# Kernel tuning notes

Measured on AMD Instinct MI355X. Metric: run time of the kernel, lower is better.

## Reference

```python
import jax, jax.numpy as jnp
import numpy as np

D_PAIR = 128
C = 128
EPS = 1e-5

def _ln(x, g, b):
    mu = jnp.mean(x, axis=-1, keepdims=True)
    var = jnp.var(x, axis=-1, keepdims=True)
    return (x - mu) * jax.lax.rsqrt(var + EPS) * g + b

def setup_inputs() -> dict:
    key = jax.random.key(0)
    ks = jax.random.split(key, 8)
    B, N, d, c = 1, 512, D_PAIR, C
    glorot = lambda k, fo, fi: jax.random.uniform(k, (fo, fi), jnp.float32,
                                                  -1.0, 1.0) * np.sqrt(6.0 / (fi + fo))
    return {
        "Z_raw": jax.random.normal(ks[0], (B, N, N, d), jnp.float32),
        "Z_mask_row": jnp.ones((B, N, N), jnp.float32),
        "ln1_g": jnp.ones((d,), jnp.float32),
        "ln1_b": jnp.zeros((d,), jnp.float32),
        "W_lr": glorot(ks[1], 2 * c, d),
        "b_lr": jnp.zeros((2 * c,), jnp.float32),
        "W_gate": jnp.zeros((2 * c, d), jnp.float32),   # initializer='zeros'
        "b_gate": jnp.ones((2 * c,), jnp.float32),      # bias_init=1.0
        "W_og": jnp.zeros((d, d), jnp.float32),
        "b_og": jnp.ones((d,), jnp.float32),
        "ln2_g": jnp.ones((c,), jnp.float32),
        "ln2_b": jnp.zeros((c,), jnp.float32),
        "W_out": jnp.zeros((d, d), jnp.float32),        # no bias
        "out_bias": jnp.zeros((d,), jnp.float32),
    }

def reference(Z_raw, Z_mask_row, ln1_g, ln1_b, W_lr, b_lr, W_gate, b_gate,
              W_og, b_og, ln2_g, ln2_b, W_out, out_bias):
    c = C
    Z = _ln(Z_raw, ln1_g, ln1_b)                         # [B,I,J,d]
    lr = jnp.einsum('bijd,ed->bije', Z, W_lr) + b_lr      # [B,I,J,2c]
    lr = Z_mask_row[..., None] * lr
    lr = lr * jax.nn.sigmoid(jnp.einsum('bijd,ed->bije', Z, W_gate) + b_gate)
    left, right = lr[..., :c], lr[..., c:]
    # triangle outgoing: p[b,i,j,c] = sum_k left[b,i,k,c] * right[b,j,k,c]
    p = jnp.einsum('bikc,bjkc->bijc', left, right)
    ab = jnp.einsum('bijc,ec->bije', _ln(p, ln2_g, ln2_b), W_out)
    g = jax.nn.sigmoid(jnp.einsum('bijd,ed->bije', Z, W_og) + b_og)
    # eval-mode bias_ele_dropout_residual (dropout mask = ones)
    return Z_raw + g * (ab + out_bias)
```

## Files before the change

### kernel.cpp

```cpp
#include <hip/hip_runtime.h>

#define NPOS 262144

typedef __attribute__((ext_vector_type(8))) short short8;
typedef __attribute__((ext_vector_type(4))) float f32x4;
typedef __attribute__((ext_vector_type(4))) unsigned short us4;
typedef __attribute__((ext_vector_type(4))) unsigned int u32x4;

__device__ __forceinline__ unsigned short f2bf(float f){
  unsigned u = __float_as_uint(f);
  u += 0x7fffu + ((u >> 16) & 1u);
  return (unsigned short)(u >> 16);
}
__device__ __forceinline__ float bf2f(unsigned int h){ return __uint_as_float(h << 16); }
__device__ __forceinline__ float sigm(float x){ return 1.f/(1.f + __expf(-x)); }

#define MFMA16(a,b,c) __builtin_amdgcn_mfma_f32_16x16x32_bf16((a),(b),(c),0,0,0)

__global__ __launch_bounds__(256) void k_prep(
    const float* __restrict__ Wlr, const float* __restrict__ b_lr,
    const float* __restrict__ Wg,  const float* __restrict__ b_g,
    const float* __restrict__ Wog, const float* __restrict__ b_og,
    const float* __restrict__ Wout,const float* __restrict__ obias,
    const float* __restrict__ g1, const float* __restrict__ b1,
    const float* __restrict__ g2, const float* __restrict__ b2,
    unsigned short* __restrict__ Wc, float* __restrict__ svec, float* __restrict__ cvec)
{
  int r = blockIdx.x*4 + (threadIdx.x >> 6);
  int l = threadIdx.x & 63;
  const float *W, *gv, *bv; float extra;
  if (r < 256)      { W = Wlr + r*128;         extra = b_lr[r];      gv=g1; bv=b1; }
  else if (r < 512) { W = Wg  + (r-256)*128;   extra = b_g[r-256];   gv=g1; bv=b1; }
  else if (r < 640) { W = Wog + (r-512)*128;   extra = b_og[r-512];  gv=g1; bv=b1; }
  else              { W = Wout+ (r-640)*128;   extra = obias[r-640]; gv=g2; bv=b2; }
  float w0 = W[2*l], w1 = W[2*l+1];
  float p0 = w0 * gv[2*l], p1 = w1 * gv[2*l+1];
  float s  = p0 + p1;
  float cc = w0 * bv[2*l] + w1 * bv[2*l+1];
  Wc[r*128 + 2*l]   = f2bf(p0);
  Wc[r*128 + 2*l+1] = f2bf(p1);
  for (int off=32; off; off>>=1){ s += __shfl_down(s, off); cc += __shfl_down(cc, off); }
  if (l == 0){ svec[r] = s; cvec[r] = cc + extra; }
}

__global__ __launch_bounds__(256) void k_proj(
    const float* __restrict__ Zraw, const float* __restrict__ Zmask,
    const unsigned short* __restrict__ Wc,
    const float* __restrict__ svec, const float* __restrict__ cvec,
    unsigned short* __restrict__ leftT, unsigned short* __restrict__ rightT)
{
  __shared__ unsigned short zt[128*144];
  __shared__ unsigned short tl[128*132];
  __shared__ float mu_s[128], rs_s[128], mask_s[128];
  __shared__ float ps[256], pss[256];
  const int t = threadIdx.x, l = t & 63, w = t >> 6;
  const int wr = w >> 1, wc = w & 1;
  const long pos0 = (long)blockIdx.x * 128;

  { const f32x4* zg = (const f32x4*)(Zraw + pos0*128);
    for (int v=0; v<16; v++){
      int f = v*256 + t, row = f>>5, c4 = f&31;
      f32x4 z = zg[f];
      us4 h; h[0]=f2bf(z[0]); h[1]=f2bf(z[1]); h[2]=f2bf(z[2]); h[3]=f2bf(z[3]);
      *(us4*)&zt[row*144 + c4*4] = h;
    }
  }
  if (t < 128) mask_s[t] = Zmask[pos0 + t];
  __syncthreads();
  {
    int sr = t & 127, hi = t >> 7;
    float s=0.f, ss=0.f;
    for (int it=hi*32; it<hi*32+32; it++){
      int c2 = (sr + it) & 63;
      unsigned u = *(const unsigned*)&zt[sr*144 + c2*2];
      float a = bf2f(u & 0xffffu), b = bf2f(u >> 16);
      s += a + b; ss += a*a + b*b;
    }
    ps[t] = s; pss[t] = ss;
  }
  __syncthreads();
  if (t < 128){
    float s = ps[t] + ps[t+128], ss = pss[t] + pss[t+128];
    float mu = s * 0.0078125f;
    float var = ss * 0.0078125f - mu*mu;
    mu_s[t] = mu; rs_s[t] = rsqrtf(var + 1e-5f);
  }
  __syncthreads();

  for (int half=0; half<2; half++){
    const unsigned short* Blr = Wc + (half*128)*128;
    const unsigned short* Bgt = Wc + (256 + half*128)*128;
    f32x4 accL[4][4], accG[4][4];
    for (int mt=0; mt<4; mt++) for (int nt=0; nt<4; nt++){
      accL[mt][nt] = (f32x4)(0.f); accG[mt][nt] = (f32x4)(0.f);
    }
    for (int ks=0; ks<4; ks++){
      const int krow = ks*32 + ((l>>4)<<3);
      short8 bl[4], bg[4];
      for (int nt=0; nt<4; nt++){
        int n = wc*64 + nt*16 + (l&15);
        bl[nt] = *(const short8*)(Blr + n*128 + krow);
        bg[nt] = *(const short8*)(Bgt + n*128 + krow);
      }
      for (int mt=0; mt<4; mt++){
        int row = wr*64 + mt*16 + (l&15);
        short8 a = *(const short8*)&zt[row*144 + krow];
        for (int nt=0; nt<4; nt++){
          accL[mt][nt] = MFMA16(a, bl[nt], accL[mt][nt]);
          accG[mt][nt] = MFMA16(a, bg[nt], accG[mt][nt]);
        }
      }
    }
    for (int mt=0; mt<4; mt++){
      int rowb = wr*64 + mt*16 + ((l>>4)<<2);
      for (int nt=0; nt<4; nt++){
        int col = wc*64 + nt*16 + (l&15);
        float sL = svec[half*128 + col],       cL = cvec[half*128 + col];
        float sG = svec[256 + half*128 + col], cG = cvec[256 + half*128 + col];
        us4 h;
        for (int r=0; r<4; r++){
          int row = rowb + r;
          float rs = rs_s[row], rm = rs*mu_s[row];
          float lrv = rs*accL[mt][nt][r] - rm*sL + cL;
          float gv  = sigm(rs*accG[mt][nt][r] - rm*sG + cG);
          h[r] = f2bf(mask_s[row] * lrv * gv);
        }
        *(us4*)&tl[col*132 + rowb] = h;
      }
    }
    __syncthreads();
    unsigned short* dst = half ? rightT : leftT;
    for (int v=0; v<32; v++){
      int f2 = v*256 + t, col = f2>>6, rp = (f2&63)<<1;
      unsigned u = *(const unsigned*)&tl[col*132 + rp];
      *(unsigned*)&dst[(long)col*NPOS + pos0 + rp] = u;
    }
    __syncthreads();
  }
}

__global__ __launch_bounds__(256) void k_tri(
    const unsigned short* __restrict__ leftT, const unsigned short* __restrict__ rightT,
    unsigned short* __restrict__ pP)
{
  __shared__ unsigned short At[128*72];
  __shared__ unsigned short Bt[128*72];
  __shared__ unsigned short pj[128*132];
  const int t = threadIdx.x, l = t & 63, w = t >> 6;
  const int wr = w >> 1, wc = w & 1;
  const int c = blockIdx.x >> 4, tile = blockIdx.x & 15;
  const int ti = (tile >> 2) << 7, tj = (tile & 3) << 7;
  const unsigned short* L = leftT  + (long)c*NPOS + (long)ti*512;
  const unsigned short* R = rightT + (long)c*NPOS + (long)tj*512;
  f32x4 acc[4][4];
  for (int mt=0; mt<4; mt++) for (int nt=0; nt<4; nt++) acc[mt][nt] = (f32x4)(0.f);
  for (int kt=0; kt<8; kt++){
    const int k0 = kt*64;
    __syncthreads();
    for (int v=0; v<4; v++){
      int f = v*256 + t, row = f>>3, kc = f&7;
      *(u32x4*)&At[row*72 + kc*8] = *(const u32x4*)(L + row*512 + k0 + kc*8);
      *(u32x4*)&Bt[row*72 + kc*8] = *(const u32x4*)(R + row*512 + k0 + kc*8);
    }
    __syncthreads();
    for (int ks2=0; ks2<2; ks2++){
      const int krow = ks2*32 + ((l>>4)<<3);
      short8 br[4];
      for (int nt=0; nt<4; nt++)
        br[nt] = *(const short8*)&Bt[(wc*64 + nt*16 + (l&15))*72 + krow];
      for (int mt=0; mt<4; mt++){
        short8 a = *(const short8*)&At[(wr*64 + mt*16 + (l&15))*72 + krow];
        for (int nt=0; nt<4; nt++)
          acc[mt][nt] = MFMA16(a, br[nt], acc[mt][nt]);
      }
    }
  }
  __syncthreads();
  for (int mt=0; mt<4; mt++){
    int rowb = wr*64 + mt*16 + ((l>>4)<<2);
    for (int nt=0; nt<4; nt++){
      int col = wc*64 + nt*16 + (l&15);
      for (int r=0; r<4; r++)
        pj[(rowb+r)*132 + col] = f2bf(acc[mt][nt][r]);
    }
  }
  __syncthreads();
  unsigned short* dst = pP + (long)c*NPOS + (long)ti*512 + tj;
  for (int v=0; v<32; v++){
    int f2 = v*256 + t, row = f2>>6, cp = (f2&63)<<1;
    unsigned u = *(const unsigned*)&pj[row*132 + cp];
    *(unsigned*)&dst[(long)row*512 + cp] = u;
  }
}

__global__ __launch_bounds__(256) void k_out(
    const float* __restrict__ Zraw, const unsigned short* __restrict__ pP,
    const unsigned short* __restrict__ Wc,
    const float* __restrict__ svec, const float* __restrict__ cvec,
    float* __restrict__ out)
{
  __shared__ unsigned short zt[128*144];
  __shared__ unsigned pt[128*65];
  __shared__ float sb[256*4];
  __shared__ float mu1s[128], rs1s[128], mu2s[128], rs2s[128];
  const int t = threadIdx.x, l = t & 63, w = t >> 6;
  const int wr = w >> 1, wc = w & 1;
  const long pos0 = (long)blockIdx.x * 128;
  const int ib = blockIdx.x >> 2, j0 = (blockIdx.x & 3) << 7;

  { const f32x4* zg = (const f32x4*)(Zraw + pos0*128);
    for (int v=0; v<16; v++){
      int f = v*256 + t, row = f>>5, c4 = f&31;
      f32x4 z = zg[f];
      us4 h; h[0]=f2bf(z[0]); h[1]=f2bf(z[1]); h[2]=f2bf(z[2]); h[3]=f2bf(z[3]);
      *(us4*)&zt[row*144 + c4*4] = h;
    }
  }
  for (int v=0; v<32; v++){
    int f = v*256 + t, cch = f>>6, j2 = f&63;
    pt[cch*65 + j2] = *(const unsigned*)&pP[(long)cch*NPOS + (long)ib*512 + j0 + 2*j2];
  }
  __syncthreads();

  {
    int sr = t & 127, hi = t >> 7;
    float s=0.f, ss=0.f;
    for (int it=hi*32; it<hi*32+32; it++){
      int c2 = (sr + it) & 63;
      unsigned u = *(const unsigned*)&zt[sr*144 + c2*2];
      float a = bf2f(u & 0xffffu), b = bf2f(u >> 16);
      s += a + b; ss += a*a + b*b;
    }
    ps_store: ;
    sb[t*4+0] = s; sb[t*4+1] = ss;
    int jp = t & 63, ch = t >> 6;
    float s0=0.f, ss0=0.f, s1=0.f, ss1=0.f;
    for (int cc=ch*32; cc<ch*32+32; cc++){
      unsigned u = pt[cc*65 + jp];
      float a = bf2f(u & 0xffffu), b = bf2f(u >> 16);
      s0 += a; ss0 += a*a; s1 += b; ss1 += b*b;
    }
    sb[t*4+2] = s0 + s1*0.f;
    __syncthreads();
    if (t < 128){
      float S = sb[t*4+0] + sb[(t+128)*4+0];
      float SS = sb[t*4+1] + sb[(t+128)*4+1];
      float mu = S*0.0078125f, var = SS*0.0078125f - mu*mu;
      mu1s[t] = mu; rs1s[t] = rsqrtf(var + 1e-5f);
    }
    __syncthreads();
    sb[t*4+0] = s0; sb[t*4+1] = ss0; sb[t*4+2] = s1; sb[t*4+3] = ss1;
    __syncthreads();
    if (t >= 128){
      int j = t - 128, jpp = j >> 1, o = j & 1;
      float S=0.f, SS=0.f;
      for (int ww=0; ww<4; ww++){
        S  += sb[(ww*64 + jpp)*4 + 2*o];
        SS += sb[(ww*64 + jpp)*4 + 2*o + 1];
      }
      float mu = S*0.0078125f, var = SS*0.0078125f - mu*mu;
      mu2s[j] = mu; rs2s[j] = rsqrtf(var + 1e-5f);
    }
  }
  __syncthreads();

  const unsigned short* W2  = Wc + 640*128;
  const unsigned short* WgB = Wc + 512*128;
  const unsigned short* pt16 = (const unsigned short*)pt;
  f32x4 acc1[4][4], acc2[4][4];
  for (int mt=0; mt<4; mt++) for (int nt=0; nt<4; nt++){
    acc1[mt][nt]=(f32x4)(0.f); acc2[mt][nt]=(f32x4)(0.f);
  }
  for (int ks=0; ks<4; ks++){
    const int krow = ks*32 + ((l>>4)<<3);
    short8 bo[4], bg[4];
    for (int nt=0; nt<4; nt++){
      int n = wc*64 + nt*16 + (l&15);
      bo[nt] = *(const short8*)(W2  + n*128 + krow);
      bg[nt] = *(const short8*)(WgB + n*128 + krow);
    }
    for (int mt=0; mt<4; mt++){
      int row = wr*64 + mt*16 + (l&15);
      short8 ap;
      #pragma unroll
      for (int m=0; m<8; m++)
        ap[m] = (short)pt16[(krow+m)*130 + row];
      short8 az = *(const short8*)&zt[row*144 + krow];
      for (int nt=0; nt<4; nt++){
        acc1[mt][nt] = MFMA16(ap, bo[nt], acc1[mt][nt]);
        acc2[mt][nt] = MFMA16(az, bg[nt], acc2[mt][nt]);
      }
    }
  }
  for (int mt=0; mt<4; mt++){
    int rowb = wr*64 + mt*16 + ((l>>4)<<2);
    for (int nt=0; nt<4; nt++){
      int col = wc*64 + nt*16 + (l&15);
      float sO = svec[640 + col], cO = cvec[640 + col];
      float sg = svec[512 + col], cg = cvec[512 + col];
      for (int r=0; r<4; r++){
        int row = rowb + r;
        float ab = rs2s[row]*acc1[mt][nt][r] - rs2s[row]*mu2s[row]*sO + cO;
        float gv = sigm(rs1s[row]*acc2[mt][nt][r] - rs1s[row]*mu1s[row]*sg + cg);
        long gidx = (pos0 + row)*128 + col;
        out[gidx] = Zraw[gidx] + gv*ab;
      }
    }
  }
}

extern "C" void kernel_launch(void* const* d_in, const int* in_sizes, int n_in,
                              void* d_out, int out_size, void* d_ws, size_t ws_size,
                              hipStream_t stream)
{
  (void)in_sizes; (void)n_in; (void)out_size; (void)ws_size;
  const float* Zraw  = (const float*)d_in[0];
  const float* Zmask = (const float*)d_in[1];
  const float* g1    = (const float*)d_in[2];
  const float* b1    = (const float*)d_in[3];
  const float* Wlr   = (const float*)d_in[4];
  const float* blr   = (const float*)d_in[5];
  const float* Wg    = (const float*)d_in[6];
  const float* bg    = (const float*)d_in[7];
  const float* Wog   = (const float*)d_in[8];
  const float* bog   = (const float*)d_in[9];
  const float* g2    = (const float*)d_in[10];
  const float* b2    = (const float*)d_in[11];
  const float* Wout  = (const float*)d_in[12];
  const float* obias = (const float*)d_in[13];

  char* ws = (char*)d_ws;
  unsigned short* leftT  = (unsigned short*)(ws);
  unsigned short* rightT = (unsigned short*)(ws + 67108864L);
  unsigned short* pP     = (unsigned short*)(ws + 134217728L);
  unsigned short* Wc     = (unsigned short*)(ws + 201326592L);
  float* svec            = (float*)(ws + 201326592L + 196608L);
  float* cvec            = (float*)(ws + 201326592L + 196608L + 4096L);
  float* out = (float*)d_out;

  k_prep<<<192, 256, 0, stream>>>(Wlr, blr, Wg, bg, Wog, bog, Wout, obias,
                                  g1, b1, g2, b2, Wc, svec, cvec);
  k_proj<<<2048, 256, 0, stream>>>(Zraw, Zmask, Wc, svec, cvec, leftT, rightT);
  k_tri<<<2048, 256, 0, stream>>>(leftT, rightT, pP);
  k_out<<<2048, 256, 0, stream>>>(Zraw, pP, Wc, svec, cvec, out);
}
```

Before: 606.0 us.

## Cut LDS and registers in proj and tri kernels, use direct global-to-LDS loads

```diff
diff --git a/kernel.cpp b/kernel.cpp
--- a/kernel.cpp
+++ b/kernel.cpp
@@ -5,7 +5,6 @@
 typedef __attribute__((ext_vector_type(8))) short short8;
 typedef __attribute__((ext_vector_type(4))) float f32x4;
 typedef __attribute__((ext_vector_type(4))) unsigned short us4;
-typedef __attribute__((ext_vector_type(4))) unsigned int u32x4;
 
 __device__ __forceinline__ unsigned short f2bf(float f){
   unsigned u = __float_as_uint(f);
@@ -16,6 +15,12 @@
 __device__ __forceinline__ float sigm(float x){ return 1.f/(1.f + __expf(-x)); }
 
 #define MFMA16(a,b,c) __builtin_amdgcn_mfma_f32_16x16x32_bf16((a),(b),(c),0,0,0)
+
+__device__ __forceinline__ void gld16(const unsigned short* g, unsigned short* l){
+  __builtin_amdgcn_global_load_lds(
+      (const __attribute__((address_space(1))) unsigned int*)g,
+      (__attribute__((address_space(3))) unsigned int*)l, 16, 0, 0);
+}
 
 __global__ __launch_bounds__(256) void k_prep(
     const float* __restrict__ Wlr, const float* __restrict__ b_lr,
@@ -43,19 +48,173 @@
   if (l == 0){ svec[r] = s; cvec[r] = cc + extra; }
 }
 
-__global__ __launch_bounds__(256) void k_proj(
+__global__ __launch_bounds__(256,3) void k_proj(
     const float* __restrict__ Zraw, const float* __restrict__ Zmask,
     const unsigned short* __restrict__ Wc,
     const float* __restrict__ svec, const float* __restrict__ cvec,
     unsigned short* __restrict__ leftT, unsigned short* __restrict__ rightT)
 {
-  __shared__ unsigned short zt[128*144];
-  __shared__ unsigned short tl[128*132];
+  __shared__ unsigned short zt[128*136];
+  __shared__ unsigned short tl[64*132];
   __shared__ float mu_s[128], rs_s[128], mask_s[128];
-  __shared__ float ps[256], pss[256];
   const int t = threadIdx.x, l = t & 63, w = t >> 6;
   const int wr = w >> 1, wc = w & 1;
   const long pos0 = (long)blockIdx.x * 128;
+
+  {
+    const float* zrow = Zraw + pos0*128 + (long)t*64;
+    const int zb = (t>>1)*136 + (t&1)*64;
+    float s = 0.f, ss = 0.f;
+    for (int v=0; v<16; v++){
+      f32x4 z = *(const f32x4*)(zrow + v*4);
+      s  += z[0]+z[1]+z[2]+z[3];
+      ss += z[0]*z[0]+z[1]*z[1]+z[2]*z[2]+z[3]*z[3];
+      us4 h; h[0]=f2bf(z[0]); h[1]=f2bf(z[1]); h[2]=f2bf(z[2]); h[3]=f2bf(z[3]);
+      *(us4*)&zt[zb + v*4] = h;
+    }
+    float S  = s  + __shfl_xor(s, 1);
+    float SS = ss + __shfl_xor(ss, 1);
+    if ((t & 1) == 0){
+      int row = t >> 1;
+      float mu = S * 0.0078125f;
+      float var = SS * 0.0078125f - mu*mu;
+      mu_s[row] = mu; rs_s[row] = rsqrtf(var + 1e-5f);
+    }
+    if (t < 128) mask_s[t] = Zmask[pos0 + t];
+  }
+  __syncthreads();
+
+  for (int half=0; half<2; half++){
+    const unsigned short* Blr = Wc + (half*128)*128;
+    const unsigned short* Bgt = Wc + (256 + half*128)*128;
+    f32x4 accL[4][4], accG[4][4];
+    for (int mt=0; mt<4; mt++) for (int nt=0; nt<4; nt++) accL[mt][nt] = (f32x4)(0.f);
+    for (int ks=0; ks<4; ks++){
+      const int krow = ks*32 + ((l>>4)<<3);
+      short8 bl[4];
+      for (int nt=0; nt<4; nt++)
+        bl[nt] = *(const short8*)(Blr + (wc*64 + nt*16 + (l&15))*128 + krow);
+      for (int mt=0; mt<4; mt++){
+        short8 a = *(const short8*)&zt[(wr*64 + mt*16 + (l&15))*136 + krow];
+        for (int nt=0; nt<4; nt++) accL[mt][nt] = MFMA16(a, bl[nt], accL[mt][nt]);
+      }
+    }
+    for (int mt=0; mt<4; mt++) for (int nt=0; nt<4; nt++) accG[mt][nt] = (f32x4)(0.f);
+    for (int ks=0; ks<4; ks++){
+      const int krow = ks*32 + ((l>>4)<<3);
+      short8 bg[4];
+      for (int nt=0; nt<4; nt++)
+        bg[nt] = *(const short8*)(Bgt + (wc*64 + nt*16 + (l&15))*128 + krow);
+      for (int mt=0; mt<4; mt++){
+        short8 a = *(const short8*)&zt[(wr*64 + mt*16 + (l&15))*136 + krow];
+        for (int nt=0; nt<4; nt++) accG[mt][nt] = MFMA16(a, bg[nt], accG[mt][nt]);
+      }
+    }
+    unsigned short* dst = half ? rightT : leftT;
+    for (int p=0; p<2; p++){
+      __syncthreads();
+      if (wc == p){
+        for (int mt=0; mt<4; mt++){
+          int rowb = wr*64 + mt*16 + ((l>>4)<<2);
+          for (int nt=0; nt<4; nt++){
+            int cloc = nt*16 + (l&15);
+            int col  = p*64 + cloc;
+            float sL = svec[half*128 + col],       cL = cvec[half*128 + col];
+            float sG = svec[256 + half*128 + col], cG = cvec[256 + half*128 + col];
+            us4 h;
+            for (int r=0; r<4; r++){
+              int row = rowb + r;
+              float rs = rs_s[row], rm = rs*mu_s[row];
+              float lrv = rs*accL[mt][nt][r] - rm*sL + cL;
+              float gv  = sigm(rs*accG[mt][nt][r] - rm*sG + cG);
+              h[r] = f2bf(mask_s[row] * lrv * gv);
+            }
+            *(us4*)&tl[cloc*132 + rowb] = h;
+          }
+        }
+      }
+      __syncthreads();
+      for (int v=0; v<16; v++){
+        int f = v*256 + t, cloc = f>>6, rp = (f&63)<<1;
+        unsigned u = *(const unsigned*)&tl[cloc*132 + rp];
+        *(unsigned*)&dst[(long)(p*64 + cloc)*NPOS + pos0 + rp] = u;
+      }
+    }
+  }
+}
+
+__global__ __launch_bounds__(256,4) void k_tri(
+    const unsigned short* __restrict__ leftT, const unsigned short* __restrict__ rightT,
+    unsigned short* __restrict__ pP)
+{
+  __shared__ __align__(16) char ldsbuf[128*132*2];
+  unsigned short* At = (unsigned short*)ldsbuf;
+  unsigned short* Bt = (unsigned short*)(ldsbuf + 8192);
+  unsigned short* pj = (unsigned short*)ldsbuf;
+  const int t = threadIdx.x, l = t & 63, w = t >> 6;
+  const int wr = w >> 1, wc = w & 1;
+  const int c = blockIdx.x >> 4, tile = blockIdx.x & 15;
+  const int ti = (tile >> 2) << 7, tj = (tile & 3) << 7;
+  const unsigned short* gA = leftT  + (long)c*NPOS + (long)(ti + w*32 + (l>>2))*512 + (l&3)*8;
+  const unsigned short* gB = rightT + (long)c*NPOS + (long)(tj + w*32 + (l>>2))*512 + (l&3)*8;
+  unsigned short* lA0 = At + (w*32)*32;
+  unsigned short* lA1 = At + (w*32+16)*32;
+  unsigned short* lB0 = Bt + (w*32)*32;
+  unsigned short* lB1 = Bt + (w*32+16)*32;
+
+  f32x4 acc[4][4];
+  for (int mt=0; mt<4; mt++) for (int nt=0; nt<4; nt++) acc[mt][nt] = (f32x4)(0.f);
+
+  for (int kt=0; kt<16; kt++){
+    const int k0 = kt*32;
+    __syncthreads();
+    gld16(gA + k0,           lA0);
+    gld16(gA + k0 + 16*512,  lA1);
+    gld16(gB + k0,           lB0);
+    gld16(gB + k0 + 16*512,  lB1);
+    __syncthreads();
+    const int krow = (l>>4)<<3;
+    short8 br[4];
+    for (int nt=0; nt<4; nt++)
+      br[nt] = *(const short8*)&Bt[(wc*64 + nt*16 + (l&15))*32 + krow];
+    for (int mt=0; mt<4; mt++){
+      short8 a = *(const short8*)&At[(wr*64 + mt*16 + (l&15))*32 + krow];
+      for (int nt=0; nt<4; nt++)
+        acc[mt][nt] = MFMA16(a, br[nt], acc[mt][nt]);
+    }
+  }
+  __syncthreads();
+  for (int mt=0; mt<4; mt++){
+    int rowb = wr*64 + mt*16 + ((l>>4)<<2);
+    for (int nt=0; nt<4; nt++){
+      int col = wc*64 + nt*16 + (l&15);
+      for (int r=0; r<4; r++)
+        pj[(rowb+r)*132 + col] = f2bf(acc[mt][nt][r]);
+    }
+  }
+  __syncthreads();
+  unsigned short* dst = pP + (long)c*NPOS + (long)ti*512 + tj;
+  for (int v=0; v<32; v++){
+    int f2 = v*256 + t, row = f2>>6, cp = (f2&63)<<1;
+    unsigned u = *(const unsigned*)&pj[row*132 + cp];
+    *(unsigned*)&dst[(long)row*512 + cp] = u;
+  }
+}
+
+__global__ __launch_bounds__(256) void k_out(
+    const float* __restrict__ Zraw, const unsigned short* __restrict__ pP,
+    const unsigned short* __restrict__ Wc,
+    const float* __restrict__ svec, const float* __restrict__ cvec,
+    float* __restrict__ out)
+{
+  __shared__ unsigned short zt[128*144];
+  __shared__ unsigned pt[128*65];
+  __shared__ float sb[256*4];
+  __shared__ float mu1s[128], rs1s[128], mu2s[128], rs2s[128];
+  const int t = threadIdx.x, l = t & 63, w = t >> 6;
+  const int wr = w >> 1, wc = w & 1;
+  const long pos0 = (long)blockIdx.x * 128;
+  const int ib = blockIdx.x >> 2, j0 = (blockIdx.x & 3) << 7;
 
   { const f32x4* zg = (const f32x4*)(Zraw + pos0*128);
     for (int v=0; v<16; v++){
@@ -65,8 +224,12 @@
       *(us4*)&zt[row*144 + c4*4] = h;
     }
   }
-  if (t < 128) mask_s[t] = Zmask[pos0 + t];
-  __syncthreads();
+  for (int v=0; v<32; v++){
+    int f = v*256 + t, cch = f>>6, j2 = f&63;
+    pt[cch*65 + j2] = *(const unsigned*)&pP[(long)cch*NPOS + (long)ib*512 + j0 + 2*j2];
+  }
+  __syncthreads();
+
   {
     int sr = t & 127, hi = t >> 7;
     float s=0.f, ss=0.f;
@@ -76,162 +239,6 @@
       float a = bf2f(u & 0xffffu), b = bf2f(u >> 16);
       s += a + b; ss += a*a + b*b;
     }
-    ps[t] = s; pss[t] = ss;
-  }
-  __syncthreads();
-  if (t < 128){
-    float s = ps[t] + ps[t+128], ss = pss[t] + pss[t+128];
-    float mu = s * 0.0078125f;
-    float var = ss * 0.0078125f - mu*mu;
-    mu_s[t] = mu; rs_s[t] = rsqrtf(var + 1e-5f);
-  }
-  __syncthreads();
-
-  for (int half=0; half<2; half++){
-    const unsigned short* Blr = Wc + (half*128)*128;
-    const unsigned short* Bgt = Wc + (256 + half*128)*128;
-    f32x4 accL[4][4], accG[4][4];
-    for (int mt=0; mt<4; mt++) for (int nt=0; nt<4; nt++){
-      accL[mt][nt] = (f32x4)(0.f); accG[mt][nt] = (f32x4)(0.f);
-    }
-    for (int ks=0; ks<4; ks++){
-      const int krow = ks*32 + ((l>>4)<<3);
-      short8 bl[4], bg[4];
-      for (int nt=0; nt<4; nt++){
-        int n = wc*64 + nt*16 + (l&15);
-        bl[nt] = *(const short8*)(Blr + n*128 + krow);
-        bg[nt] = *(const short8*)(Bgt + n*128 + krow);
-      }
-      for (int mt=0; mt<4; mt++){
-        int row = wr*64 + mt*16 + (l&15);
-        short8 a = *(const short8*)&zt[row*144 + krow];
-        for (int nt=0; nt<4; nt++){
-          accL[mt][nt] = MFMA16(a, bl[nt], accL[mt][nt]);
-          accG[mt][nt] = MFMA16(a, bg[nt], accG[mt][nt]);
-        }
-      }
-    }
-    for (int mt=0; mt<4; mt++){
-      int rowb = wr*64 + mt*16 + ((l>>4)<<2);
-      for (int nt=0; nt<4; nt++){
-        int col = wc*64 + nt*16 + (l&15);
-        float sL = svec[half*128 + col],       cL = cvec[half*128 + col];
-        float sG = svec[256 + half*128 + col], cG = cvec[256 + half*128 + col];
-        us4 h;
-        for (int r=0; r<4; r++){
-          int row = rowb + r;
-          float rs = rs_s[row], rm = rs*mu_s[row];
-          float lrv = rs*accL[mt][nt][r] - rm*sL + cL;
-          float gv  = sigm(rs*accG[mt][nt][r] - rm*sG + cG);
-          h[r] = f2bf(mask_s[row] * lrv * gv);
-        }
-        *(us4*)&tl[col*132 + rowb] = h;
-      }
-    }
-    __syncthreads();
-    unsigned short* dst = half ? rightT : leftT;
-    for (int v=0; v<32; v++){
-      int f2 = v*256 + t, col = f2>>6, rp = (f2&63)<<1;
-      unsigned u = *(const unsigned*)&tl[col*132 + rp];
-      *(unsigned*)&dst[(long)col*NPOS + pos0 + rp] = u;
-    }
-    __syncthreads();
-  }
-}
-
-__global__ __launch_bounds__(256) void k_tri(
-    const unsigned short* __restrict__ leftT, const unsigned short* __restrict__ rightT,
-    unsigned short* __restrict__ pP)
-{
-  __shared__ unsigned short At[128*72];
-  __shared__ unsigned short Bt[128*72];
-  __shared__ unsigned short pj[128*132];
-  const int t = threadIdx.x, l = t & 63, w = t >> 6;
-  const int wr = w >> 1, wc = w & 1;
-  const int c = blockIdx.x >> 4, tile = blockIdx.x & 15;
-  const int ti = (tile >> 2) << 7, tj = (tile & 3) << 7;
-  const unsigned short* L = leftT  + (long)c*NPOS + (long)ti*512;
-  const unsigned short* R = rightT + (long)c*NPOS + (long)tj*512;
-  f32x4 acc[4][4];
-  for (int mt=0; mt<4; mt++) for (int nt=0; nt<4; nt++) acc[mt][nt] = (f32x4)(0.f);
-  for (int kt=0; kt<8; kt++){
-    const int k0 = kt*64;
-    __syncthreads();
-    for (int v=0; v<4; v++){
-      int f = v*256 + t, row = f>>3, kc = f&7;
-      *(u32x4*)&At[row*72 + kc*8] = *(const u32x4*)(L + row*512 + k0 + kc*8);
-      *(u32x4*)&Bt[row*72 + kc*8] = *(const u32x4*)(R + row*512 + k0 + kc*8);
-    }
-    __syncthreads();
-    for (int ks2=0; ks2<2; ks2++){
-      const int krow = ks2*32 + ((l>>4)<<3);
-      short8 br[4];
-      for (int nt=0; nt<4; nt++)
-        br[nt] = *(const short8*)&Bt[(wc*64 + nt*16 + (l&15))*72 + krow];
-      for (int mt=0; mt<4; mt++){
-        short8 a = *(const short8*)&At[(wr*64 + mt*16 + (l&15))*72 + krow];
-        for (int nt=0; nt<4; nt++)
-          acc[mt][nt] = MFMA16(a, br[nt], acc[mt][nt]);
-      }
-    }
-  }
-  __syncthreads();
-  for (int mt=0; mt<4; mt++){
-    int rowb = wr*64 + mt*16 + ((l>>4)<<2);
-    for (int nt=0; nt<4; nt++){
-      int col = wc*64 + nt*16 + (l&15);
-      for (int r=0; r<4; r++)
-        pj[(rowb+r)*132 + col] = f2bf(acc[mt][nt][r]);
-    }
-  }
-  __syncthreads();
-  unsigned short* dst = pP + (long)c*NPOS + (long)ti*512 + tj;
-  for (int v=0; v<32; v++){
-    int f2 = v*256 + t, row = f2>>6, cp = (f2&63)<<1;
-    unsigned u = *(const unsigned*)&pj[row*132 + cp];
-    *(unsigned*)&dst[(long)row*512 + cp] = u;
-  }
-}
-
-__global__ __launch_bounds__(256) void k_out(
-    const float* __restrict__ Zraw, const unsigned short* __restrict__ pP,
-    const unsigned short* __restrict__ Wc,
-    const float* __restrict__ svec, const float* __restrict__ cvec,
-    float* __restrict__ out)
-{
-  __shared__ unsigned short zt[128*144];
-  __shared__ unsigned pt[128*65];
-  __shared__ float sb[256*4];
-  __shared__ float mu1s[128], rs1s[128], mu2s[128], rs2s[128];
-  const int t = threadIdx.x, l = t & 63, w = t >> 6;
-  const int wr = w >> 1, wc = w & 1;
-  const long pos0 = (long)blockIdx.x * 128;
-  const int ib = blockIdx.x >> 2, j0 = (blockIdx.x & 3) << 7;
-
-  { const f32x4* zg = (const f32x4*)(Zraw + pos0*128);
-    for (int v=0; v<16; v++){
-      int f = v*256 + t, row = f>>5, c4 = f&31;
-      f32x4 z = zg[f];
-      us4 h; h[0]=f2bf(z[0]); h[1]=f2bf(z[1]); h[2]=f2bf(z[2]); h[3]=f2bf(z[3]);
-      *(us4*)&zt[row*144 + c4*4] = h;
-    }
-  }
-  for (int v=0; v<32; v++){
-    int f = v*256 + t, cch = f>>6, j2 = f&63;
-    pt[cch*65 + j2] = *(const unsigned*)&pP[(long)cch*NPOS + (long)ib*512 + j0 + 2*j2];
-  }
-  __syncthreads();
-
-  {
-    int sr = t & 127, hi = t >> 7;
-    float s=0.f, ss=0.f;
-    for (int it=hi*32; it<hi*32+32; it++){
-      int c2 = (sr + it) & 63;
-      unsigned u = *(const unsigned*)&zt[sr*144 + c2*2];
-      float a = bf2f(u & 0xffffu), b = bf2f(u >> 16);
-      s += a + b; ss += a*a + b*b;
-    }
-    ps_store: ;
     sb[t*4+0] = s; sb[t*4+1] = ss;
     int jp = t & 63, ch = t >> 6;
     float s0=0.f, ss0=0.f, s1=0.f, ss1=0.f;
@@ -240,7 +247,6 @@
       float a = bf2f(u & 0xffffu), b = bf2f(u >> 16);
       s0 += a; ss0 += a*a; s1 += b; ss1 += b*b;
     }
-    sb[t*4+2] = s0 + s1*0.f;
     __syncthreads();
     if (t < 128){
       float S = sb[t*4+0] + sb[(t+128)*4+0];
```

Result: slower. 810.1 us (+33.7%).
